# Optimization experiments

Hardware: AMD Instinct MI355X
Metric: run time of the kernel (lower is better)

Reference implementation:

```python
import jax, jax.numpy as jnp
import numpy as np

DIM = 1024
N_HEADS = 16
HEAD_DIM = DIM // N_HEADS
HIDDEN = 4096
EPS = 1e-12


def setup_inputs() -> dict:
    key = jax.random.key(0)
    ks = jax.random.split(key, 12)
    B, S = 2, 2048
    s = 0.02
    inp = {
        "x": jax.random.normal(ks[0], (B, S, DIM), jnp.float32),
        "attn_mask": jnp.ones((B, S), jnp.int32),
        "Wq": jax.random.normal(ks[1], (DIM, DIM), jnp.float32) * s,
        "bq": jnp.zeros((DIM,), jnp.float32),
        "Wk": jax.random.normal(ks[2], (DIM, DIM), jnp.float32) * s,
        "bk": jnp.zeros((DIM,), jnp.float32),
        "Wv": jax.random.normal(ks[3], (DIM, DIM), jnp.float32) * s,
        "bv": jnp.zeros((DIM,), jnp.float32),
        "Wo": jax.random.normal(ks[4], (DIM, DIM), jnp.float32) * s,
        "bo": jnp.zeros((DIM,), jnp.float32),
        "ln1_g": jnp.ones((DIM,), jnp.float32),
        "ln1_b": jnp.zeros((DIM,), jnp.float32),
        "W1": jax.random.normal(ks[5], (DIM, HIDDEN), jnp.float32) * s,
        "b1": jnp.zeros((HIDDEN,), jnp.float32),
        "W2": jax.random.normal(ks[6], (HIDDEN, DIM), jnp.float32) * s,
        "b2": jnp.zeros((DIM,), jnp.float32),
        "ln2_g": jnp.ones((DIM,), jnp.float32),
        "ln2_b": jnp.zeros((DIM,), jnp.float32),
    }
    return inp


def _layernorm(x, g, b):
    mu = jnp.mean(x, axis=-1, keepdims=True)
    var = jnp.mean(jnp.square(x - mu), axis=-1, keepdims=True)
    return (x - mu) * jax.lax.rsqrt(var + EPS) * g + b


def reference(x, attn_mask, Wq, bq, Wk, bk, Wv, bv, Wo, bo,
              ln1_g, ln1_b, W1, b1, W2, b2, ln2_g, ln2_b):
    B, S, D = x.shape
    def split_heads(t):  # (B,S,D) -> (B,H,S,hd)
        return t.reshape(B, S, N_HEADS, HEAD_DIM).transpose(0, 2, 1, 3)
    q = split_heads(x @ Wq + bq) * (1.0 / np.sqrt(HEAD_DIM))
    k = split_heads(x @ Wk + bk)
    v = split_heads(x @ Wv + bv)
    scores = jnp.einsum("bhqd,bhkd->bhqk", q, k)  # (B,H,S,S)
    neg = jnp.finfo(scores.dtype).min
    mask = (attn_mask == 0)[:, None, None, :]  # (B,1,1,S)
    scores = jnp.where(mask, neg, scores)
    weights = jax.nn.softmax(scores, axis=-1)
    ctx = jnp.einsum("bhqk,bhkd->bhqd", weights, v)
    ctx = ctx.transpose(0, 2, 1, 3).reshape(B, S, D)
    sa_out = ctx @ Wo + bo
    sa_out = _layernorm(sa_out + x, ln1_g, ln1_b)
    h = jax.nn.gelu(sa_out @ W1 + b1, approximate=False)
    ffn_out = h @ W2 + b2
    out = _layernorm(ffn_out + sa_out, ln2_g, ln2_b)
    return out
```

## Files before the change

### kernel.cpp

```cpp
#include <hip/hip_runtime.h>


typedef __bf16 bf16x8 __attribute__((ext_vector_type(8)));
typedef __bf16 bf16x4v __attribute__((ext_vector_type(4)));
typedef float f32x4 __attribute__((ext_vector_type(4)));

#define DIM_ 1024
#define S_LEN 2048
#define NH 16

__device__ __forceinline__ unsigned short f2bf(float f) {
  unsigned u = __float_as_uint(f);
  u = (u + 0x7FFFu + ((u >> 16) & 1u)) >> 16;
  return (unsigned short)u;
}
__device__ __forceinline__ float bf2f(unsigned short h) {
  return __uint_as_float(((unsigned)h) << 16);
}
__device__ __forceinline__ f32x4 mfma16(bf16x8 a, bf16x8 b, f32x4 c) {
  return __builtin_amdgcn_mfma_f32_16x16x32_bf16(a, b, c, 0, 0, 0);
}
__device__ __forceinline__ void gload_lds16(const void* g, void* l) {
  __builtin_amdgcn_global_load_lds(
      (const __attribute__((address_space(1))) void*)g,
      (__attribute__((address_space(3))) void*)l, 16, 0, 0);
}
__device__ __forceinline__ int swz(int row) { return ((row ^ (row >> 3)) & 7) << 3; }

__global__ __launch_bounds__(256) void trans_cvt(
    const float* __restrict__ W, unsigned short* __restrict__ Wt, int K, int N)
{
  __shared__ float tile[64][65];
  const int n0 = blockIdx.x * 64, k0 = blockIdx.y * 64;
  const int tid = threadIdx.x;
  const int tr = tid >> 4, tc = (tid & 15) << 2;
#pragma unroll
  for (int rr = 0; rr < 64; rr += 16) {
    const float4 v = *(const float4*)&W[(size_t)(k0 + tr + rr) * N + n0 + tc];
    tile[tr + rr][tc + 0] = v.x; tile[tr + rr][tc + 1] = v.y;
    tile[tr + rr][tc + 2] = v.z; tile[tr + rr][tc + 3] = v.w;
  }
  __syncthreads();
#pragma unroll
  for (int nn = 0; nn < 64; nn += 16) {
    const int n = tr + nn;
    ushort4 o;
    o.x = f2bf(tile[tc + 0][n]);
    o.y = f2bf(tile[tc + 1][n]);
    o.z = f2bf(tile[tc + 2][n]);
    o.w = f2bf(tile[tc + 3][n]);
    *(ushort4*)&Wt[(size_t)(n0 + n) * K + k0 + tc] = o;
  }
}

__global__ void cvt_bf16(const float* __restrict__ in,
                         unsigned short* __restrict__ out, int n4)
{
  const int i = blockIdx.x * blockDim.x + threadIdx.x;
  if (i >= n4) return;
  const float4 v = ((const float4*)in)[i];
  ushort4 o = { f2bf(v.x), f2bf(v.y), f2bf(v.z), f2bf(v.w) };
  ((ushort4*)out)[i] = o;
}

__global__ __launch_bounds__(256) void trans_v(
    const unsigned short* __restrict__ v, unsigned short* __restrict__ vt)
{
  __shared__ unsigned short tile[64][66];
  const int st = blockIdx.x, bh = blockIdx.y;
  const int tid = threadIdx.x;
  const int r = tid >> 3, c = (tid & 7) << 3;
  const size_t base = (size_t)bh * (S_LEN * 64);
#pragma unroll
  for (int p = 0; p < 2; ++p) {
    const int s = r + p * 32;
    const uint4 raw = *(const uint4*)(v + base + (size_t)(st * 64 + s) * 64 + c);
    const unsigned short* pr = (const unsigned short*)&raw;
#pragma unroll
    for (int j = 0; j < 8; ++j) tile[s][c + j] = pr[j];
  }
  __syncthreads();
#pragma unroll
  for (int p = 0; p < 2; ++p) {
    const int hd = r + p * 32;
    ushort4 o[2];
#pragma unroll
    for (int j = 0; j < 8; ++j) ((unsigned short*)o)[j] = tile[c + j][hd];
    *(uint4*)(vt + (size_t)bh * (64 * S_LEN) + (size_t)hd * S_LEN + st * 64 + c) =
        *(const uint4*)o;
  }
}

template <int EPI>
__global__ __launch_bounds__(256) void gemm_bt(
    const unsigned short* __restrict__ A,
    const unsigned short* __restrict__ Bt,
    const float* __restrict__ bias,
    const float* __restrict__ bias2,
    const float* __restrict__ bias3,
    int N, int K,
    unsigned short* __restrict__ bout)
{
  __shared__ __align__(16) unsigned short As[128 * 64];
  __shared__ __align__(16) unsigned short Bs[128 * 64];
  const int tn = blockIdx.x, tm = blockIdx.y;
  const int tid = threadIdx.x;
  const int wid = tid >> 6, lane = tid & 63;
  const int wm = wid >> 1, wn = wid & 1;
  const int l15 = lane & 15, lg = lane >> 4;
  const int srow = lane >> 3, sk8 = (lane & 7) << 3;

  f32x4 acc[4][4];
#pragma unroll
  for (int i = 0; i < 4; ++i)
#pragma unroll
    for (int j = 0; j < 4; ++j) acc[i][j] = (f32x4){0.f, 0.f, 0.f, 0.f};

  const size_t abase = (size_t)(tm * 128) * K;
  const size_t bbase = (size_t)(tn * 128) * K;

  for (int kk = 0; kk < K; kk += 64) {
    __syncthreads();
#pragma unroll
    for (int s = 0; s < 4; ++s) {
      const int row = wid * 32 + s * 8 + srow;
      const int sw = sk8 ^ swz(row);
      gload_lds16(A + abase + (size_t)row * K + kk + sw, &As[(wid * 32 + s * 8) * 64]);
      gload_lds16(Bt + bbase + (size_t)row * K + kk + sw, &Bs[(wid * 32 + s * 8) * 64]);
    }
    __syncthreads();
#pragma unroll
    for (int sub = 0; sub < 2; ++sub) {
      bf16x8 af[4], bfr[4];
#pragma unroll
      for (int mr = 0; mr < 4; ++mr) {
        const int row = wm * 64 + mr * 16 + l15;
        af[mr] = *(const bf16x8*)&As[row * 64 + ((sub * 32 + lg * 8) ^ swz(row))];
      }
#pragma unroll
      for (int nr = 0; nr < 4; ++nr) {
        const int row = wn * 64 + nr * 16 + l15;
        bfr[nr] = *(const bf16x8*)&Bs[row * 64 + ((sub * 32 + lg * 8) ^ swz(row))];
      }
#pragma unroll
      for (int mr = 0; mr < 4; ++mr)
#pragma unroll
        for (int nr = 0; nr < 4; ++nr)
          acc[mr][nr] = mfma16(af[mr], bfr[nr], acc[mr][nr]);
    }
  }

#pragma unroll
  for (int nr = 0; nr < 4; ++nr) {
    const int col = tn * 128 + wn * 64 + nr * 16 + l15;
    float bv;
    int which = 0, c = col;
    if (EPI == 0) {
      which = col >> 10;
      c = col & 1023;
      const float* bp = (which == 0) ? bias : (which == 1) ? bias2 : bias3;
      bv = bp[c];
    } else {
      bv = bias[col];
    }
#pragma unroll
    for (int mr = 0; mr < 4; ++mr) {
#pragma unroll
      for (int j = 0; j < 4; ++j) {
        const int row = tm * 128 + wm * 64 + mr * 16 + lg * 4 + j;
        float v = acc[mr][nr][j] + bv;
        if (EPI == 0) {
          if (which == 0) v *= 0.125f;
          const int b = row >> 11, s = row & 2047, h = c >> 6, hd = c & 63;
          bout[(size_t)which * 4194304 +
               (((size_t)(b * NH + h)) * S_LEN + s) * 64 + hd] = f2bf(v);
        } else {
          const float gl = 0.5f * v * (1.f + erff(v * 0.70710678118654752f));
          bout[(size_t)row * N + col] = f2bf(gl);
        }
      }
    }
  }
}

template <int EPI>
__global__ __launch_bounds__(256) void gemm64(
    const unsigned short* __restrict__ A,
    const unsigned short* __restrict__ Bt,
    const float* __restrict__ bias,
    int N, int K,
    float* __restrict__ fout,
    const float* __restrict__ resf,
    const unsigned short* __restrict__ resb)
{
  __shared__ __align__(16) unsigned short As[2][64 * 64];
  __shared__ __align__(16) unsigned short Bs[2][128 * 64];
  const int tn = blockIdx.x, tm = blockIdx.y;
  const int tid = threadIdx.x;
  const int wid = tid >> 6, lane = tid & 63;
  const int wm = wid >> 1, wn = wid & 1;
  const int l15 = lane & 15, lg = lane >> 4;
  const int srow = lane >> 3, sk8 = (lane & 7) << 3;

  f32x4 acc[2][4];
#pragma unroll
  for (int i = 0; i < 2; ++i)
#pragma unroll
    for (int j = 0; j < 4; ++j) acc[i][j] = (f32x4){0.f, 0.f, 0.f, 0.f};

  const size_t abase = (size_t)(tm * 64) * K;
  const size_t bbase = (size_t)(tn * 128) * K;

  auto STAGE = [&](int bufn, int kk) {
#pragma unroll
    for (int s = 0; s < 2; ++s) {
      const int row = wid * 16 + s * 8 + srow;
      gload_lds16(A + abase + (size_t)row * K + kk + (sk8 ^ swz(row)),
                  &As[bufn][(wid * 16 + s * 8) * 64]);
    }
#pragma unroll
    for (int s = 0; s < 4; ++s) {
      const int row = wid * 32 + s * 8 + srow;
      gload_lds16(Bt + bbase + (size_t)row * K + kk + (sk8 ^ swz(row)),
                  &Bs[bufn][(wid * 32 + s * 8) * 64]);
    }
  };

  STAGE(0, 0);
  __syncthreads();
  int cur = 0;
  for (int kk = 0; kk < K; kk += 64) {
    if (kk + 64 < K) STAGE(cur ^ 1, kk + 64);
#pragma unroll
    for (int sub = 0; sub < 2; ++sub) {
      bf16x8 af[2], bfr[4];
#pragma unroll
      for (int mr = 0; mr < 2; ++mr) {
        const int row = wm * 32 + mr * 16 + l15;
        af[mr] = *(const bf16x8*)&As[cur][row * 64 + ((sub * 32 + lg * 8) ^ swz(row))];
      }
#pragma unroll
      for (int nr = 0; nr < 4; ++nr) {
        const int row = wn * 64 + nr * 16 + l15;
        bfr[nr] = *(const bf16x8*)&Bs[cur][row * 64 + ((sub * 32 + lg * 8) ^ swz(row))];
      }
#pragma unroll
      for (int mr = 0; mr < 2; ++mr)
#pragma unroll
        for (int nr = 0; nr < 4; ++nr)
          acc[mr][nr] = mfma16(af[mr], bfr[nr], acc[mr][nr]);
    }
    __syncthreads();
    cur ^= 1;
  }

#pragma unroll
  for (int nr = 0; nr < 4; ++nr) {
    const int col = tn * 128 + wn * 64 + nr * 16 + l15;
    const float bv = bias[col];
#pragma unroll
    for (int mr = 0; mr < 2; ++mr) {
#pragma unroll
      for (int j = 0; j < 4; ++j) {
        const int row = tm * 64 + wm * 32 + mr * 16 + lg * 4 + j;
        const float v = acc[mr][nr][j] + bv;
        if (EPI == 1) {
          fout[(size_t)row * N + col] = v + resf[(size_t)row * N + col];
        } else {
          fout[(size_t)row * N + col] = v + bf2f(resb[(size_t)row * N + col]);
        }
      }
    }
  }
}

__global__ __launch_bounds__(512) void attn_fwd(
    const unsigned short* __restrict__ qg,
    const unsigned short* __restrict__ kg,
    const unsigned short* __restrict__ vtg,
    const int* __restrict__ amask,
    unsigned short* __restrict__ ctx)
{
  __shared__ __align__(16) unsigned short Ks[2][64 * 64];
  __shared__ __align__(16) unsigned short Vs[2][64 * 64];
  __shared__ __align__(16) unsigned short Ps[8][16 * 72];
  __shared__ __align__(16) int mk[2][64];

  const int bx = blockIdx.x;
  const int qt = (bx >> 3) & 15;
  const int bh = ((bx & 7) << 2) | (bx >> 7);
  const int b = bh >> 4, h = bh & 15;
  const int tid = threadIdx.x;
  const int wid = tid >> 6, lane = tid & 63;
  const int l15 = lane & 15, lg = lane >> 4;
  const int srow = lane >> 3, sk8 = (lane & 7) << 3;

  const size_t qoff =
      (((size_t)bh * S_LEN) + qt * 128 + wid * 16 + l15) * 64 + lg * 8;
  const bf16x8 aq0 = *(const bf16x8*)&qg[qoff];
  const bf16x8 aq1 = *(const bf16x8*)&qg[qoff + 32];

  f32x4 o_[4];
#pragma unroll
  for (int n = 0; n < 4; ++n) o_[n] = (f32x4){0.f, 0.f, 0.f, 0.f};
  float mreg = -3e38f, lsum = 0.f;

  const size_t kbase  = (size_t)bh * (S_LEN * 64);
  const size_t vtbase = (size_t)bh * (64 * S_LEN);
  unsigned short* Pw = &Ps[wid][0];
  const int rk = wid * 8 + srow;
  const int swr = sk8 ^ swz(rk);

  auto STAGE = [&](int bufn, int t) {
    gload_lds16(kg + kbase + (size_t)(t * 64 + rk) * 64 + swr,
                &Ks[bufn][wid * 8 * 64]);
    gload_lds16(vtg + vtbase + (size_t)rk * S_LEN + t * 64 + swr,
                &Vs[bufn][wid * 8 * 64]);
    if (tid < 64) mk[bufn][tid] = amask[b * S_LEN + t * 64 + tid];
  };

  STAGE(0, 0);
  __syncthreads();
  int cur = 0;

  for (int t = 0; t < S_LEN / 64; ++t) {
    if (t + 1 < S_LEN / 64) STAGE(cur ^ 1, t + 1);

    __builtin_amdgcn_s_setprio(1);
    f32x4 sf[4];
#pragma unroll
    for (int nr = 0; nr < 4; ++nr) {
      const int kvloc = nr * 16 + l15;
      const int e = swz(kvloc);
      const bf16x8 bk0 = *(const bf16x8*)&Ks[cur][kvloc * 64 + ((lg * 8) ^ e)];
      const bf16x8 bk1 = *(const bf16x8*)&Ks[cur][kvloc * 64 + ((32 + lg * 8) ^ e)];
      f32x4 a = (f32x4){0.f, 0.f, 0.f, 0.f};
      a = mfma16(bk0, aq0, a);
      a = mfma16(bk1, aq1, a);
      sf[nr] = a;
    }
    __builtin_amdgcn_s_setprio(0);

#pragma unroll
    for (int nr = 0; nr < 4; ++nr) {
      const int4 mki = *(const int4*)&mk[cur][nr * 16 + lg * 4];
      if (mki.x == 0) sf[nr][0] = -3e38f;
      if (mki.y == 0) sf[nr][1] = -3e38f;
      if (mki.z == 0) sf[nr][2] = -3e38f;
      if (mki.w == 0) sf[nr][3] = -3e38f;
    }

    float pmax = fmaxf(fmaxf(fmaxf(sf[0][0], sf[0][1]), fmaxf(sf[0][2], sf[0][3])),
                       fmaxf(fmaxf(sf[1][0], sf[1][1]), fmaxf(sf[1][2], sf[1][3])));
    pmax = fmaxf(pmax,
           fmaxf(fmaxf(fmaxf(sf[2][0], sf[2][1]), fmaxf(sf[2][2], sf[2][3])),
                 fmaxf(fmaxf(sf[3][0], sf[3][1]), fmaxf(sf[3][2], sf[3][3]))));
    pmax = fmaxf(pmax, __shfl_xor(pmax, 16));
    pmax = fmaxf(pmax, __shfl_xor(pmax, 32));

    if (__any(pmax > mreg + 8.f)) {
      const float mn = fmaxf(mreg, pmax);
      const float sc = __expf(mreg - mn);
      mreg = mn;
      lsum *= sc;
      float scr[4];
#pragma unroll
      for (int j = 0; j < 4; ++j) scr[j] = __shfl(sc, lg * 4 + j);
#pragma unroll
      for (int n = 0; n < 4; ++n) {
        o_[n][0] *= scr[0]; o_[n][1] *= scr[1];
        o_[n][2] *= scr[2]; o_[n][3] *= scr[3];
      }
    }

    asm volatile("s_waitcnt lgkmcnt(0)" ::: "memory");
#pragma unroll
    for (int nr = 0; nr < 4; ++nr) {
      const float p0 = __expf(sf[nr][0] - mreg);
      const float p1 = __expf(sf[nr][1] - mreg);
      const float p2 = __expf(sf[nr][2] - mreg);
      const float p3 = __expf(sf[nr][3] - mreg);
      lsum += (p0 + p1) + (p2 + p3);
      bf16x4v pk;
      pk[0] = (__bf16)p0; pk[1] = (__bf16)p1;
      pk[2] = (__bf16)p2; pk[3] = (__bf16)p3;
      *(bf16x4v*)&Pw[l15 * 72 + nr * 16 + lg * 4] = pk;
    }
    asm volatile("s_waitcnt lgkmcnt(0)" ::: "memory");

    __builtin_amdgcn_s_setprio(1);
    {
      const bf16x8 pa0 = *(const bf16x8*)&Pw[l15 * 72 + lg * 8];
      const bf16x8 pa1 = *(const bf16x8*)&Pw[l15 * 72 + 32 + lg * 8];
#pragma unroll
      for (int n = 0; n < 4; ++n) {
        const int hd = n * 16 + l15;
        const int eh = swz(hd);
        const bf16x8 bv0 = *(const bf16x8*)&Vs[cur][hd * 64 + ((lg * 8) ^ eh)];
        const bf16x8 bv1 = *(const bf16x8*)&Vs[cur][hd * 64 + ((32 + lg * 8) ^ eh)];
        o_[n] = mfma16(pa0, bv0, o_[n]);
        o_[n] = mfma16(pa1, bv1, o_[n]);
      }
    }
    __builtin_amdgcn_s_setprio(0);
    __syncthreads();
    cur ^= 1;
  }

  lsum += __shfl_xor(lsum, 16);
  lsum += __shfl_xor(lsum, 32);
  const float rinv = 1.f / lsum;
  float rj[4];
#pragma unroll
  for (int j = 0; j < 4; ++j) rj[j] = __shfl(rinv, lg * 4 + j);
#pragma unroll
  for (int n = 0; n < 4; ++n) {
#pragma unroll
    for (int j = 0; j < 4; ++j) {
      const int sr = qt * 128 + wid * 16 + lg * 4 + j;
      const size_t idx = ((size_t)b * S_LEN + sr) * DIM_ + h * 64 + n * 16 + l15;
      ctx[idx] = f2bf(o_[n][j] * rj[j]);
    }
  }
}

template <int OUTBF>
__global__ __launch_bounds__(256) void ln_fused(
    const float* __restrict__ in, const float* __restrict__ g,
    const float* __restrict__ be,
    float* __restrict__ fout, unsigned short* __restrict__ bout)
{
  const int row = blockIdx.x, tid = threadIdx.x;
  const float4 v = ((const float4*)(in + (size_t)row * DIM_))[tid];
  float s = v.x + v.y + v.z + v.w;
  float s2 = v.x * v.x + v.y * v.y + v.z * v.z + v.w * v.w;
#pragma unroll
  for (int off = 1; off < 64; off <<= 1) {
    s += __shfl_xor(s, off);
    s2 += __shfl_xor(s2, off);
  }
  __shared__ float rs[4], rs2[4];
  if ((tid & 63) == 0) { rs[tid >> 6] = s; rs2[tid >> 6] = s2; }
  __syncthreads();
  s  = rs[0] + rs[1] + rs[2] + rs[3];
  s2 = rs2[0] + rs2[1] + rs2[2] + rs2[3];
  const float mean = s * (1.f / DIM_);
  const float var = fmaxf(s2 * (1.f / DIM_) - mean * mean, 0.f);
  const float inv = rsqrtf(var + 1e-12f);
  const float4 gv = ((const float4*)g)[tid];
  const float4 bv = ((const float4*)be)[tid];
  const float o0 = (v.x - mean) * inv * gv.x + bv.x;
  const float o1 = (v.y - mean) * inv * gv.y + bv.y;
  const float o2 = (v.z - mean) * inv * gv.z + bv.z;
  const float o3 = (v.w - mean) * inv * gv.w + bv.w;
  if (OUTBF) {
    ushort4 o = { f2bf(o0), f2bf(o1), f2bf(o2), f2bf(o3) };
    ((ushort4*)(bout + (size_t)row * DIM_))[tid] = o;
  } else {
    ((float4*)(fout + (size_t)row * DIM_))[tid] = make_float4(o0, o1, o2, o3);
  }
}

extern "C" void kernel_launch(void* const* d_in, const int* in_sizes, int n_in,
                              void* d_out, int out_size, void* d_ws, size_t ws_size,
                              hipStream_t stream)
{
  const float* x   = (const float*)d_in[0];
  const int* amask = (const int*)d_in[1];
  const float* Wq  = (const float*)d_in[2];
  const float* bq  = (const float*)d_in[3];
  const float* Wk  = (const float*)d_in[4];
  const float* bk  = (const float*)d_in[5];
  const float* Wv  = (const float*)d_in[6];
  const float* bv  = (const float*)d_in[7];
  const float* Wo  = (const float*)d_in[8];
  const float* bo  = (const float*)d_in[9];
  const float* g1  = (const float*)d_in[10];
  const float* be1 = (const float*)d_in[11];
  const float* W1  = (const float*)d_in[12];
  const float* b1  = (const float*)d_in[13];
  const float* W2  = (const float*)d_in[14];
  const float* b2  = (const float*)d_in[15];
  const float* g2  = (const float*)d_in[16];
  const float* be2 = (const float*)d_in[17];
  float* out = (float*)d_out;

  char* ws = (char*)d_ws;
  const size_t MB = (size_t)1 << 20;
  unsigned short* wqkvT = (unsigned short*)(ws + 0 * MB);
  unsigned short* wqt = wqkvT;
  unsigned short* wkt = (unsigned short*)(ws + 2 * MB);
  unsigned short* wvt = (unsigned short*)(ws + 4 * MB);
  unsigned short* wot = (unsigned short*)(ws + 6 * MB);
  unsigned short* w1t = (unsigned short*)(ws + 8 * MB);
  unsigned short* w2t = (unsigned short*)(ws + 16 * MB);
  unsigned short* qb  = (unsigned short*)(ws + 24 * MB);
  unsigned short* xb  = (unsigned short*)(ws + 48 * MB);
  unsigned short* vtb = (unsigned short*)(ws + 48 * MB);
  unsigned short* ctx = (unsigned short*)(ws + 56 * MB);
  unsigned short* sab = qb;
  unsigned short* hb  = (unsigned short*)(ws + 32 * MB);
  float* preln = out;

  trans_cvt<<<dim3(16, 16), 256, 0, stream>>>(Wq, wqt, 1024, 1024);
  trans_cvt<<<dim3(16, 16), 256, 0, stream>>>(Wk, wkt, 1024, 1024);
  trans_cvt<<<dim3(16, 16), 256, 0, stream>>>(Wv, wvt, 1024, 1024);
  trans_cvt<<<dim3(16, 16), 256, 0, stream>>>(Wo, wot, 1024, 1024);
  trans_cvt<<<dim3(64, 16), 256, 0, stream>>>(W1, w1t, 1024, 4096);
  trans_cvt<<<dim3(16, 64), 256, 0, stream>>>(W2, w2t, 4096, 1024);
  cvt_bf16<<<4096, 256, 0, stream>>>(x, xb, 4096 * 1024 / 4);

  gemm_bt<0><<<dim3(24, 32), 256, 0, stream>>>(xb, wqkvT, bq, bk, bv,
      3072, 1024, qb);

  trans_v<<<dim3(32, 32), 256, 0, stream>>>(qb + 2 * 4194304, vtb);

  attn_fwd<<<512, 512, 0, stream>>>(qb, qb + 4194304, vtb, amask, ctx);

  gemm64<1><<<dim3(8, 64), 256, 0, stream>>>(ctx, wot, bo, 1024, 1024,
      preln, x, nullptr);
  ln_fused<1><<<4096, 256, 0, stream>>>(preln, g1, be1, nullptr, sab);

  gemm_bt<2><<<dim3(32, 32), 256, 0, stream>>>(sab, w1t, b1, nullptr, nullptr,
      4096, 1024, hb);
  gemm64<3><<<dim3(8, 64), 256, 0, stream>>>(hb, w2t, b2, 1024, 4096,
      preln, nullptr, sab);
  ln_fused<0><<<4096, 256, 0, stream>>>(preln, g2, be2, out, nullptr);
}
```

Before: 395.4 us.

## Unify GEMMs into double-buffered 64x128 kernel and batch weight transposes

The QKV and FFN1 GEMMs move from a single-buffered 128x128 tile kernel to the double-buffered 64x128 kernel the other GEMMs already used. One templated kernel now covers all epilogues, and the grid doubles along M. Overlapping the next tile's global-to-LDS load with MFMA work is meant to hide memory latency and give more blocks per launch, at the cost of less reuse per tile. The four square weight transposes are also merged into one launch via blockIdx.z to cut launch overhead.

```diff
diff --git a/kernel.cpp b/kernel.cpp
--- a/kernel.cpp
+++ b/kernel.cpp
@@ -27,9 +27,16 @@
 }
 __device__ __forceinline__ int swz(int row) { return ((row ^ (row >> 3)) & 7) << 3; }
 
-__global__ __launch_bounds__(256) void trans_cvt(
-    const float* __restrict__ W, unsigned short* __restrict__ Wt, int K, int N)
-{
+__global__ __launch_bounds__(256) void trans_cvt4(
+    const float* __restrict__ Wa, const float* __restrict__ Wb,
+    const float* __restrict__ Wc, const float* __restrict__ Wd,
+    unsigned short* __restrict__ Ta, unsigned short* __restrict__ Tb,
+    unsigned short* __restrict__ Tc, unsigned short* __restrict__ Td)
+{
+  const int z = blockIdx.z;
+  const float* W = (z == 0) ? Wa : (z == 1) ? Wb : (z == 2) ? Wc : Wd;
+  unsigned short* Wt = (z == 0) ? Ta : (z == 1) ? Tb : (z == 2) ? Tc : Td;
+  const int K = 1024, N = 1024;
   __shared__ float tile[64][65];
   const int n0 = blockIdx.x * 64, k0 = blockIdx.y * 64;
   const int tid = threadIdx.x;
@@ -53,6 +60,32 @@
   }
 }
 
+__global__ __launch_bounds__(256) void trans_cvt(
+    const float* __restrict__ W, unsigned short* __restrict__ Wt, int K, int N)
+{
+  __shared__ float tile[64][65];
+  const int n0 = blockIdx.x * 64, k0 = blockIdx.y * 64;
+  const int tid = threadIdx.x;
+  const int tr = tid >> 4, tc = (tid & 15) << 2;
+#pragma unroll
+  for (int rr = 0; rr < 64; rr += 16) {
+    const float4 v = *(const float4*)&W[(size_t)(k0 + tr + rr) * N + n0 + tc];
+    tile[tr + rr][tc + 0] = v.x; tile[tr + rr][tc + 1] = v.y;
+    tile[tr + rr][tc + 2] = v.z; tile[tr + rr][tc + 3] = v.w;
+  }
+  __syncthreads();
+#pragma unroll
+  for (int nn = 0; nn < 64; nn += 16) {
+    const int n = tr + nn;
+    ushort4 o;
+    o.x = f2bf(tile[tc + 0][n]);
+    o.y = f2bf(tile[tc + 1][n]);
+    o.z = f2bf(tile[tc + 2][n]);
+    o.w = f2bf(tile[tc + 3][n]);
+    *(ushort4*)&Wt[(size_t)(n0 + n) * K + k0 + tc] = o;
+  }
+}
+
 __global__ void cvt_bf16(const float* __restrict__ in,
                          unsigned short* __restrict__ out, int n4)
 {
@@ -92,17 +125,20 @@
 }
 
 template <int EPI>
-__global__ __launch_bounds__(256) void gemm_bt(
+__global__ __launch_bounds__(256) void gemmdb(
     const unsigned short* __restrict__ A,
     const unsigned short* __restrict__ Bt,
     const float* __restrict__ bias,
     const float* __restrict__ bias2,
     const float* __restrict__ bias3,
     int N, int K,
-    unsigned short* __restrict__ bout)
-{
-  __shared__ __align__(16) unsigned short As[128 * 64];
-  __shared__ __align__(16) unsigned short Bs[128 * 64];
+    float* __restrict__ fout,
+    unsigned short* __restrict__ bout,
+    const float* __restrict__ resf,
+    const unsigned short* __restrict__ resb)
+{
+  __shared__ __align__(16) unsigned short As[2][64 * 64];
+  __shared__ __align__(16) unsigned short Bs[2][128 * 64];
   const int tn = blockIdx.x, tm = blockIdx.y;
   const int tid = threadIdx.x;
   const int wid = tid >> 6, lane = tid & 63;
@@ -110,44 +146,56 @@
   const int l15 = lane & 15, lg = lane >> 4;
   const int srow = lane >> 3, sk8 = (lane & 7) << 3;
 
-  f32x4 acc[4][4];
-#pragma unroll
-  for (int i = 0; i < 4; ++i)
+  f32x4 acc[2][4];
+#pragma unroll
+  for (int i = 0; i < 2; ++i)
 #pragma unroll
     for (int j = 0; j < 4; ++j) acc[i][j] = (f32x4){0.f, 0.f, 0.f, 0.f};
 
-  const size_t abase = (size_t)(tm * 128) * K;
+  const size_t abase = (size_t)(tm * 64) * K;
   const size_t bbase = (size_t)(tn * 128) * K;
 
-  for (int kk = 0; kk < K; kk += 64) {
-    __syncthreads();
+  auto STAGE = [&](int bufn, int kk) {
+#pragma unroll
+    for (int s = 0; s < 2; ++s) {
+      const int row = wid * 16 + s * 8 + srow;
+      gload_lds16(A + abase + (size_t)row * K + kk + (sk8 ^ swz(row)),
+                  &As[bufn][(wid * 16 + s * 8) * 64]);
+    }
 #pragma unroll
     for (int s = 0; s < 4; ++s) {
       const int row = wid * 32 + s * 8 + srow;
-      const int sw = sk8 ^ swz(row);
-      gload_lds16(A + abase + (size_t)row * K + kk + sw, &As[(wid * 32 + s * 8) * 64]);
-      gload_lds16(Bt + bbase + (size_t)row * K + kk + sw, &Bs[(wid * 32 + s * 8) * 64]);
-    }
-    __syncthreads();
+      gload_lds16(Bt + bbase + (size_t)row * K + kk + (sk8 ^ swz(row)),
+                  &Bs[bufn][(wid * 32 + s * 8) * 64]);
+    }
+  };
+
+  STAGE(0, 0);
+  __syncthreads();
+  int cur = 0;
+  for (int kk = 0; kk < K; kk += 64) {
+    if (kk + 64 < K) STAGE(cur ^ 1, kk + 64);
 #pragma unroll
     for (int sub = 0; sub < 2; ++sub) {
-      bf16x8 af[4], bfr[4];
-#pragma unroll
-      for (int mr = 0; mr < 4; ++mr) {
-        const int row = wm * 64 + mr * 16 + l15;
-        af[mr] = *(const bf16x8*)&As[row * 64 + ((sub * 32 + lg * 8) ^ swz(row))];
+      bf16x8 af[2], bfr[4];
+#pragma unroll
+      for (int mr = 0; mr < 2; ++mr) {
+        const int row = wm * 32 + mr * 16 + l15;
+        af[mr] = *(const bf16x8*)&As[cur][row * 64 + ((sub * 32 + lg * 8) ^ swz(row))];
       }
 #pragma unroll
       for (int nr = 0; nr < 4; ++nr) {
         const int row = wn * 64 + nr * 16 + l15;
-        bfr[nr] = *(const bf16x8*)&Bs[row * 64 + ((sub * 32 + lg * 8) ^ swz(row))];
+        bfr[nr] = *(const bf16x8*)&Bs[cur][row * 64 + ((sub * 32 + lg * 8) ^ swz(row))];
       }
 #pragma unroll
-      for (int mr = 0; mr < 4; ++mr)
+      for (int mr = 0; mr < 2; ++mr)
 #pragma unroll
         for (int nr = 0; nr < 4; ++nr)
           acc[mr][nr] = mfma16(af[mr], bfr[nr], acc[mr][nr]);
     }
+    __syncthreads();
+    cur ^= 1;
   }
 
 #pragma unroll
@@ -164,108 +212,21 @@
       bv = bias[col];
     }
 #pragma unroll
-    for (int mr = 0; mr < 4; ++mr) {
+    for (int mr = 0; mr < 2; ++mr) {
 #pragma unroll
       for (int j = 0; j < 4; ++j) {
-        const int row = tm * 128 + wm * 64 + mr * 16 + lg * 4 + j;
+        const int row = tm * 64 + wm * 32 + mr * 16 + lg * 4 + j;
         float v = acc[mr][nr][j] + bv;
         if (EPI == 0) {
           if (which == 0) v *= 0.125f;
           const int b = row >> 11, s = row & 2047, h = c >> 6, hd = c & 63;
           bout[(size_t)which * 4194304 +
                (((size_t)(b * NH + h)) * S_LEN + s) * 64 + hd] = f2bf(v);
-        } else {
+        } else if (EPI == 1) {
+          fout[(size_t)row * N + col] = v + resf[(size_t)row * N + col];
+        } else if (EPI == 2) {
           const float gl = 0.5f * v * (1.f + erff(v * 0.70710678118654752f));
           bout[(size_t)row * N + col] = f2bf(gl);
-        }
-      }
-    }
-  }
-}
-
-template <int EPI>
-__global__ __launch_bounds__(256) void gemm64(
-    const unsigned short* __restrict__ A,
-    const unsigned short* __restrict__ Bt,
-    const float* __restrict__ bias,
-    int N, int K,
-    float* __restrict__ fout,
-    const float* __restrict__ resf,
-    const unsigned short* __restrict__ resb)
-{
-  __shared__ __align__(16) unsigned short As[2][64 * 64];
-  __shared__ __align__(16) unsigned short Bs[2][128 * 64];
-  const int tn = blockIdx.x, tm = blockIdx.y;
-  const int tid = threadIdx.x;
-  const int wid = tid >> 6, lane = tid & 63;
-  const int wm = wid >> 1, wn = wid & 1;
-  const int l15 = lane & 15, lg = lane >> 4;
-  const int srow = lane >> 3, sk8 = (lane & 7) << 3;
-
-  f32x4 acc[2][4];
-#pragma unroll
-  for (int i = 0; i < 2; ++i)
-#pragma unroll
-    for (int j = 0; j < 4; ++j) acc[i][j] = (f32x4){0.f, 0.f, 0.f, 0.f};
-
-  const size_t abase = (size_t)(tm * 64) * K;
-  const size_t bbase = (size_t)(tn * 128) * K;
-
-  auto STAGE = [&](int bufn, int kk) {
-#pragma unroll
-    for (int s = 0; s < 2; ++s) {
-      const int row = wid * 16 + s * 8 + srow;
-      gload_lds16(A + abase + (size_t)row * K + kk + (sk8 ^ swz(row)),
-                  &As[bufn][(wid * 16 + s * 8) * 64]);
-    }
-#pragma unroll
-    for (int s = 0; s < 4; ++s) {
-      const int row = wid * 32 + s * 8 + srow;
-      gload_lds16(Bt + bbase + (size_t)row * K + kk + (sk8 ^ swz(row)),
-                  &Bs[bufn][(wid * 32 + s * 8) * 64]);
-    }
-  };
-
-  STAGE(0, 0);
-  __syncthreads();
-  int cur = 0;
-  for (int kk = 0; kk < K; kk += 64) {
-    if (kk + 64 < K) STAGE(cur ^ 1, kk + 64);
-#pragma unroll
-    for (int sub = 0; sub < 2; ++sub) {
-      bf16x8 af[2], bfr[4];
-#pragma unroll
-      for (int mr = 0; mr < 2; ++mr) {
-        const int row = wm * 32 + mr * 16 + l15;
-        af[mr] = *(const bf16x8*)&As[cur][row * 64 + ((sub * 32 + lg * 8) ^ swz(row))];
-      }
-#pragma unroll
-      for (int nr = 0; nr < 4; ++nr) {
-        const int row = wn * 64 + nr * 16 + l15;
-        bfr[nr] = *(const bf16x8*)&Bs[cur][row * 64 + ((sub * 32 + lg * 8) ^ swz(row))];
-      }
-#pragma unroll
-      for (int mr = 0; mr < 2; ++mr)
-#pragma unroll
-        for (int nr = 0; nr < 4; ++nr)
-          acc[mr][nr] = mfma16(af[mr], bfr[nr], acc[mr][nr]);
-    }
-    __syncthreads();
-    cur ^= 1;
-  }
-
-#pragma unroll
-  for (int nr = 0; nr < 4; ++nr) {
-    const int col = tn * 128 + wn * 64 + nr * 16 + l15;
-    const float bv = bias[col];
-#pragma unroll
-    for (int mr = 0; mr < 2; ++mr) {
-#pragma unroll
-      for (int j = 0; j < 4; ++j) {
-        const int row = tm * 64 + wm * 32 + mr * 16 + lg * 4 + j;
-        const float v = acc[mr][nr][j] + bv;
-        if (EPI == 1) {
-          fout[(size_t)row * N + col] = v + resf[(size_t)row * N + col];
         } else {
           fout[(size_t)row * N + col] = v + bf2f(resb[(size_t)row * N + col]);
         }
@@ -502,28 +463,26 @@
   unsigned short* hb  = (unsigned short*)(ws + 32 * MB);
   float* preln = out;
 
-  trans_cvt<<<dim3(16, 16), 256, 0, stream>>>(Wq, wqt, 1024, 1024);
-  trans_cvt<<<dim3(16, 16), 256, 0, stream>>>(Wk, wkt, 1024, 1024);
-  trans_cvt<<<dim3(16, 16), 256, 0, stream>>>(Wv, wvt, 1024, 1024);
-  trans_cvt<<<dim3(16, 16), 256, 0, stream>>>(Wo, wot, 1024, 1024);
+  trans_cvt4<<<dim3(16, 16, 4), 256, 0, stream>>>(Wq, Wk, Wv, Wo,
+                                                  wqt, wkt, wvt, wot);
   trans_cvt<<<dim3(64, 16), 256, 0, stream>>>(W1, w1t, 1024, 4096);
   trans_cvt<<<dim3(16, 64), 256, 0, stream>>>(W2, w2t, 4096, 1024);
   cvt_bf16<<<4096, 256, 0, stream>>>(x, xb, 4096 * 1024 / 4);
 
-  gemm_bt<0><<<dim3(24, 32), 256, 0, stream>>>(xb, wqkvT, bq, bk, bv,
-      3072, 1024, qb);
+  gemmdb<0><<<dim3(24, 64), 256, 0, stream>>>(xb, wqkvT, bq, bk, bv,
+      3072, 1024, nullptr, qb, nullptr, nullptr);
 
   trans_v<<<dim3(32, 32), 256, 0, stream>>>(qb + 2 * 4194304, vtb);
 
   attn_fwd<<<512, 512, 0, stream>>>(qb, qb + 4194304, vtb, amask, ctx);
 
-  gemm64<1><<<dim3(8, 64), 256, 0, stream>>>(ctx, wot, bo, 1024, 1024,
-      preln, x, nullptr);
+  gemmdb<1><<<dim3(8, 64), 256, 0, stream>>>(ctx, wot, bo, nullptr, nullptr,
+      1024, 1024, preln, nullptr, x, nullptr);
   ln_fused<1><<<4096, 256, 0, stream>>>(preln, g1, be1, nullptr, sab);
 
-  gemm_bt<2><<<dim3(32, 32), 256, 0, stream>>>(sab, w1t, b1, nullptr, nullptr,
-      4096, 1024, hb);
-  gemm64<3><<<dim3(8, 64), 256, 0, stream>>>(hb, w2t, b2, 1024, 4096,
-      preln, nullptr, sab);
+  gemmdb<2><<<dim3(32, 64), 256, 0, stream>>>(sab, w1t, b1, nullptr, nullptr,
+      4096, 1024, nullptr, hb, nullptr, nullptr);
+  gemmdb<3><<<dim3(8, 64), 256, 0, stream>>>(hb, w2t, b2, nullptr, nullptr,
+      1024, 4096, preln, nullptr, nullptr, sab);
   ln_fused<0><<<4096, 256, 0, stream>>>(preln, g2, be2, out, nullptr);
 }
```

Result: faster. 379.9 us (-3.9%).

## Double-buffer LDS in 128-tile GEMM and batch four weight transposes

Applied to the files above, without the earlier changes.

The 128x128 GEMM used for the QKV and FFN1 projections now keeps two LDS buffers. It issues the async global-to-LDS load for the next K tile before computing on the current one, with one barrier per iteration instead of two, so load latency overlaps the MFMA work. Separately, the four 1024x1024 weight transpose-and-convert launches are merged into one launch with a z-dimension selecting the matrix, which cuts launch overhead. The double buffer doubles LDS use per block to 64KB, which may reduce occupancy.

```diff
diff --git a/kernel.cpp b/kernel.cpp
--- a/kernel.cpp
+++ b/kernel.cpp
@@ -27,9 +27,16 @@
 }
 __device__ __forceinline__ int swz(int row) { return ((row ^ (row >> 3)) & 7) << 3; }
 
-__global__ __launch_bounds__(256) void trans_cvt(
-    const float* __restrict__ W, unsigned short* __restrict__ Wt, int K, int N)
-{
+__global__ __launch_bounds__(256) void trans_cvt4(
+    const float* __restrict__ Wa, const float* __restrict__ Wb,
+    const float* __restrict__ Wc, const float* __restrict__ Wd,
+    unsigned short* __restrict__ Ta, unsigned short* __restrict__ Tb,
+    unsigned short* __restrict__ Tc, unsigned short* __restrict__ Td)
+{
+  const int z = blockIdx.z;
+  const float* W = (z == 0) ? Wa : (z == 1) ? Wb : (z == 2) ? Wc : Wd;
+  unsigned short* Wt = (z == 0) ? Ta : (z == 1) ? Tb : (z == 2) ? Tc : Td;
+  const int K = 1024, N = 1024;
   __shared__ float tile[64][65];
   const int n0 = blockIdx.x * 64, k0 = blockIdx.y * 64;
   const int tid = threadIdx.x;
@@ -53,6 +60,32 @@
   }
 }
 
+__global__ __launch_bounds__(256) void trans_cvt(
+    const float* __restrict__ W, unsigned short* __restrict__ Wt, int K, int N)
+{
+  __shared__ float tile[64][65];
+  const int n0 = blockIdx.x * 64, k0 = blockIdx.y * 64;
+  const int tid = threadIdx.x;
+  const int tr = tid >> 4, tc = (tid & 15) << 2;
+#pragma unroll
+  for (int rr = 0; rr < 64; rr += 16) {
+    const float4 v = *(const float4*)&W[(size_t)(k0 + tr + rr) * N + n0 + tc];
+    tile[tr + rr][tc + 0] = v.x; tile[tr + rr][tc + 1] = v.y;
+    tile[tr + rr][tc + 2] = v.z; tile[tr + rr][tc + 3] = v.w;
+  }
+  __syncthreads();
+#pragma unroll
+  for (int nn = 0; nn < 64; nn += 16) {
+    const int n = tr + nn;
+    ushort4 o;
+    o.x = f2bf(tile[tc + 0][n]);
+    o.y = f2bf(tile[tc + 1][n]);
+    o.z = f2bf(tile[tc + 2][n]);
+    o.w = f2bf(tile[tc + 3][n]);
+    *(ushort4*)&Wt[(size_t)(n0 + n) * K + k0 + tc] = o;
+  }
+}
+
 __global__ void cvt_bf16(const float* __restrict__ in,
                          unsigned short* __restrict__ out, int n4)
 {
@@ -92,7 +125,7 @@
 }
 
 template <int EPI>
-__global__ __launch_bounds__(256) void gemm_bt(
+__global__ __launch_bounds__(256) void gemm128(
     const unsigned short* __restrict__ A,
     const unsigned short* __restrict__ Bt,
     const float* __restrict__ bias,
@@ -101,8 +134,8 @@
     int N, int K,
     unsigned short* __restrict__ bout)
 {
-  __shared__ __align__(16) unsigned short As[128 * 64];
-  __shared__ __align__(16) unsigned short Bs[128 * 64];
+  __shared__ __align__(16) unsigned short As[2][128 * 64];
+  __shared__ __align__(16) unsigned short Bs[2][128 * 64];
   const int tn = blockIdx.x, tm = blockIdx.y;
   const int tid = threadIdx.x;
   const int wid = tid >> 6, lane = tid & 63;
@@ -119,28 +152,35 @@
   const size_t abase = (size_t)(tm * 128) * K;
   const size_t bbase = (size_t)(tn * 128) * K;
 
-  for (int kk = 0; kk < K; kk += 64) {
-    __syncthreads();
+  auto STAGE = [&](int bufn, int kk) {
 #pragma unroll
     for (int s = 0; s < 4; ++s) {
       const int row = wid * 32 + s * 8 + srow;
       const int sw = sk8 ^ swz(row);
-      gload_lds16(A + abase + (size_t)row * K + kk + sw, &As[(wid * 32 + s * 8) * 64]);
-      gload_lds16(Bt + bbase + (size_t)row * K + kk + sw, &Bs[(wid * 32 + s * 8) * 64]);
-    }
-    __syncthreads();
+      gload_lds16(A + abase + (size_t)row * K + kk + sw,
+                  &As[bufn][(wid * 32 + s * 8) * 64]);
+      gload_lds16(Bt + bbase + (size_t)row * K + kk + sw,
+                  &Bs[bufn][(wid * 32 + s * 8) * 64]);
+    }
+  };
+
+  STAGE(0, 0);
+  __syncthreads();
+  int cur = 0;
+  for (int kk = 0; kk < K; kk += 64) {
+    if (kk + 64 < K) STAGE(cur ^ 1, kk + 64);
 #pragma unroll
     for (int sub = 0; sub < 2; ++sub) {
       bf16x8 af[4], bfr[4];
 #pragma unroll
       for (int mr = 0; mr < 4; ++mr) {
         const int row = wm * 64 + mr * 16 + l15;
-        af[mr] = *(const bf16x8*)&As[row * 64 + ((sub * 32 + lg * 8) ^ swz(row))];
+        af[mr] = *(const bf16x8*)&As[cur][row * 64 + ((sub * 32 + lg * 8) ^ swz(row))];
       }
 #pragma unroll
       for (int nr = 0; nr < 4; ++nr) {
         const int row = wn * 64 + nr * 16 + l15;
-        bfr[nr] = *(const bf16x8*)&Bs[row * 64 + ((sub * 32 + lg * 8) ^ swz(row))];
+        bfr[nr] = *(const bf16x8*)&Bs[cur][row * 64 + ((sub * 32 + lg * 8) ^ swz(row))];
       }
 #pragma unroll
       for (int mr = 0; mr < 4; ++mr)
@@ -148,6 +188,8 @@
         for (int nr = 0; nr < 4; ++nr)
           acc[mr][nr] = mfma16(af[mr], bfr[nr], acc[mr][nr]);
     }
+    __syncthreads();
+    cur ^= 1;
   }
 
 #pragma unroll
@@ -184,7 +226,7 @@
 }
 
 template <int EPI>
-__global__ __launch_bounds__(256) void gemm64(
+__global__ __launch_bounds__(256) void gemmdb(
     const unsigned short* __restrict__ A,
     const unsigned short* __restrict__ Bt,
     const float* __restrict__ bias,
@@ -502,28 +544,26 @@
   unsigned short* hb  = (unsigned short*)(ws + 32 * MB);
   float* preln = out;
 
-  trans_cvt<<<dim3(16, 16), 256, 0, stream>>>(Wq, wqt, 1024, 1024);
-  trans_cvt<<<dim3(16, 16), 256, 0, stream>>>(Wk, wkt, 1024, 1024);
-  trans_cvt<<<dim3(16, 16), 256, 0, stream>>>(Wv, wvt, 1024, 1024);
-  trans_cvt<<<dim3(16, 16), 256, 0, stream>>>(Wo, wot, 1024, 1024);
+  trans_cvt4<<<dim3(16, 16, 4), 256, 0, stream>>>(Wq, Wk, Wv, Wo,
+                                                  wqt, wkt, wvt, wot);
   trans_cvt<<<dim3(64, 16), 256, 0, stream>>>(W1, w1t, 1024, 4096);
   trans_cvt<<<dim3(16, 64), 256, 0, stream>>>(W2, w2t, 4096, 1024);
   cvt_bf16<<<4096, 256, 0, stream>>>(x, xb, 4096 * 1024 / 4);
 
-  gemm_bt<0><<<dim3(24, 32), 256, 0, stream>>>(xb, wqkvT, bq, bk, bv,
+  gemm128<0><<<dim3(24, 32), 256, 0, stream>>>(xb, wqkvT, bq, bk, bv,
       3072, 1024, qb);
 
   trans_v<<<dim3(32, 32), 256, 0, stream>>>(qb + 2 * 4194304, vtb);
 
   attn_fwd<<<512, 512, 0, stream>>>(qb, qb + 4194304, vtb, amask, ctx);
 
-  gemm64<1><<<dim3(8, 64), 256, 0, stream>>>(ctx, wot, bo, 1024, 1024,
+  gemmdb<1><<<dim3(8, 64), 256, 0, stream>>>(ctx, wot, bo, 1024, 1024,
       preln, x, nullptr);
   ln_fused<1><<<4096, 256, 0, stream>>>(preln, g1, be1, nullptr, sab);
 
-  gemm_bt<2><<<dim3(32, 32), 256, 0, stream>>>(sab, w1t, b1, nullptr, nullptr,
+  gemm128<2><<<dim3(32, 32), 256, 0, stream>>>(sab, w1t, b1, nullptr, nullptr,
       4096, 1024, hb);
-  gemm64<3><<<dim3(8, 64), 256, 0, stream>>>(hb, w2t, b2, 1024, 4096,
+  gemmdb<3><<<dim3(8, 64), 256, 0, stream>>>(hb, w2t, b2, 1024, 4096,
       preln, nullptr, sab);
   ln_fused<0><<<4096, 256, 0, stream>>>(preln, g2, be2, out, nullptr);
 }
```

Result: faster. 374.6 us (-5.3%).
